# Optimization experiments

Measured on AMD Instinct MI355X. Metric: run time of the kernel, lower is better.

Reference implementation:

```python
import jax, jax.numpy as jnp
import numpy as np
from math import sqrt

BS, SEQ, NV, DM, K = 16, 1024, 512, 256, 8
EPS = 0.05  # sinkhorn epsilon
TEMP = 0.07  # concrete-bernoulli temperature


def setup_inputs() -> dict:
    key = jax.random.key(0)
    k1, k2, k3 = jax.random.split(key, 3)
    x = jax.random.normal(k1, (BS, SEQ, NV), jnp.float32)
    # nn.Linear(seq_len, d_model): weight [d_model, seq_len], bias [d_model]
    W = jax.random.normal(k2, (DM, SEQ), jnp.float32) / sqrt(SEQ)
    b = jnp.zeros((DM,), jnp.float32)
    cluster_emb = jax.random.normal(k3, (K, DM), jnp.float32) / sqrt(DM)
    return {"x": x, "W": W, "b": b, "cluster_emb": cluster_emb}


def _l2norm(z):
    # F.normalize(x, dim=1, p=2) with eps=1e-12 clamp
    n = jnp.maximum(jnp.linalg.norm(z, axis=1, keepdims=True), 1e-12)
    return z / n


def _sinkhorn(q):
    Q = jnp.exp(q / EPS)
    return Q / jnp.sum(Q, axis=1, keepdims=True)


def _concrete_bern(p, key):
    u = jax.random.uniform(key, p.shape, p.dtype, 1e-10, 1.0 - 1e-10)
    noise = jnp.log(u) - jnp.log1p(-u)
    logit = jnp.log(p + 1e-10) - jnp.log(1.0 - p + 1e-10)
    return jax.nn.sigmoid((logit + noise) / TEMP)


def _forward(x, W, b, cluster_emb):
    bs, S, nv = x.shape
    d = W.shape[0]
    k = cluster_emb.shape[0]
    # permute -> [bs, nv, S], Linear(S -> d)
    x_emb = jnp.einsum('bsv,ds->bvd', x, W) + b  # [bs, nv, d]
    x_flat = x_emb.reshape(-1, d)  # [bs*nv, d]
    # cosine-similarity cluster logits
    prob = (_l2norm(x_flat) @ _l2norm(cluster_emb).T).reshape(bs, nv, k)
    prob_temp = _sinkhorn(prob.reshape(-1, k)).reshape(bs, nv, k)  # individual probs
    prob_avg = _sinkhorn(jnp.mean(prob, axis=0))  # [nv, k]
    mask = _concrete_bern(prob_avg, jax.random.key(42))  # [nv, k]
    # CrossAttention with n_heads=1 (dropout inactive in eval)
    scale = 1.0 / sqrt(d)
    scores = jnp.einsum('kd,bvd->bkv', cluster_emb, x_emb)  # [bs, k, nv]
    A = jax.nn.softmax(scale * scores, axis=-1) * mask.T[None]  # masked attn
    V = jnp.einsum('bkv,bvd->bkd', A, x_emb)  # [bs, k, d]
    cluster_emb_avg = jnp.mean(V, axis=0)  # [k, d] (stored attribute in torch)
    # cluster_base_encoding: straight-through bernoulli, broadcast over seq_len
    soft = prob_temp.transpose(2, 0, 1)[..., None]  # [k, bs, nv, 1]
    u = jax.random.uniform(jax.random.key(7), soft.shape, soft.dtype)
    bern = (u < jax.lax.stop_gradient(soft)).astype(soft.dtype)
    extend = jnp.broadcast_to(bern, (k, bs, nv, S))  # [k, bs, nv, S]
    hard = soft + jax.lax.stop_gradient(extend - soft)  # straight-through
    return hard


def reference(x, W, b, cluster_emb):
    return _forward(x, W, b, cluster_emb)
```

## Files before the change

### kernel.cpp

```cpp
#include <hip/hip_runtime.h>
#include <math.h>
#include <stdint.h>

#define BS 16
#define SEQ 1024
#define NV 512
#define DM 256
#define NK 8

__device__ double g_WC[NK * SEQ];
__device__ double g_Bk[NK];
__device__ __align__(16) float g_Wt[SEQ * DM];
__device__ __align__(16) float g_zp[4 * BS * NV * DM];
__device__ double g_nn2[BS * NV];
__device__ double g_Dp[8 * BS * NV * NK];
__device__ unsigned char g_bits[BS * NV];

__device__ __forceinline__ void threefry2x32_key7(uint32_t x0, uint32_t x1,
                                                  uint32_t& o0, uint32_t& o1) {
    const uint32_t k0 = 0u, k1 = 7u;
    const uint32_t k2 = k0 ^ k1 ^ 0x1BD11BDAu;
    uint32_t v0 = x0 + k0, v1 = x1 + k1;
#define TF_ROUND(r) { v0 += v1; v1 = (v1 << (r)) | (v1 >> (32 - (r))); v1 ^= v0; }
    TF_ROUND(13) TF_ROUND(15) TF_ROUND(26) TF_ROUND(6)
    v0 += k1; v1 += k2 + 1u;
    TF_ROUND(17) TF_ROUND(29) TF_ROUND(16) TF_ROUND(24)
    v0 += k2; v1 += k0 + 2u;
    TF_ROUND(13) TF_ROUND(15) TF_ROUND(26) TF_ROUND(6)
    v0 += k0; v1 += k1 + 3u;
    TF_ROUND(17) TF_ROUND(29) TF_ROUND(16) TF_ROUND(24)
    v0 += k1; v1 += k2 + 4u;
    TF_ROUND(13) TF_ROUND(15) TF_ROUND(26) TF_ROUND(6)
    v0 += k2; v1 += k0 + 5u;
#undef TF_ROUND
    o0 = v0; o1 = v1;
}

__device__ __forceinline__ float bits_to_uniform(uint32_t b) {
    return __uint_as_float((b >> 9) | 0x3F800000u) - 1.0f;
}

__device__ __forceinline__ void cp16(const float* g, float* l) {
    __builtin_amdgcn_global_load_lds(
        (const __attribute__((address_space(1))) void*)g,
        (__attribute__((address_space(3))) void*)l,
        16, 0, 0);
}

__global__ __launch_bounds__(256) void prep_merged_kernel(
        const float* __restrict__ W, const float* __restrict__ bias,
        const float* __restrict__ ce) {
    __shared__ float tile[64][132];
    __shared__ double red[256];
    __shared__ double cen[256];
    const int t = threadIdx.x;
    const int bid = blockIdx.x;

    if (bid < 32) {
        const int s0 = (bid & 15) * 64;
        const int d0 = (bid >> 4) * 128;
#pragma unroll
        for (int p = 0; p < 32; ++p) {
            int lin = p * 256 + t;
            int d = lin >> 6, s = lin & 63;
            tile[s][d] = W[(size_t)(d0 + d) * SEQ + s0 + s];
        }
        __syncthreads();
#pragma unroll
        for (int p = 0; p < 32; ++p) {
            int lin = p * 256 + t;
            int s = lin >> 7, d = lin & 127;
            g_Wt[(size_t)(s0 + s) * DM + d0 + d] = tile[s][d];
        }
        return;
    }

    const int pid = bid - 32;
    const int k = pid >> 2;
    const int schunk = pid & 3;

    double c = (double)ce[k * DM + t];
    red[t] = c * c;
    __syncthreads();
    for (int off = 128; off > 0; off >>= 1) {
        if (t < off) red[t] += red[t + off];
        __syncthreads();
    }
    double nc = fmax(sqrt(red[0]), 1e-12);
    cen[t] = c / nc;
    __syncthreads();
    red[t] = (double)bias[t] * cen[t];
    __syncthreads();
    for (int off = 128; off > 0; off >>= 1) {
        if (t < off) red[t] += red[t + off];
        __syncthreads();
    }
    if (t == 0 && schunk == 0) g_Bk[k] = red[0];

    const int s = schunk * 256 + t;
    double acc = 0.0;
#pragma unroll 8
    for (int d = 0; d < DM; ++d)
        acc += cen[d] * (double)W[(size_t)d * SEQ + s];
    g_WC[(size_t)k * SEQ + s] = acc;
}

#define KC 32

__global__ __launch_bounds__(256) void gemm_kernel(
        const float* __restrict__ x) {
    __shared__ __align__(16) float wst[2][KC * 256];

    const int t = threadIdx.x;
    const int kblk = blockIdx.x;
    const int vblk = blockIdx.y;
    const int b    = blockIdx.z;
    const int v0 = vblk * 64;
    const float* xb = x + (size_t)b * SEQ * NV + v0;

    const int tv8 = (t & 7) * 8;
    const int td8 = (t >> 3) * 8;
    const int w = t >> 6;
    const int l = t & 63;

    const int wrow0 = w * 8;
    const size_t g_lane4 = (size_t)l * 4;

    float acc[8][8];
#pragma unroll
    for (int j = 0; j < 8; ++j)
#pragma unroll
        for (int i = 0; i < 8; ++i) acc[j][i] = 0.0f;

#define STAGE(BUF, S0)                                                         \
    {                                                                          \
        _Pragma("unroll")                                                      \
        for (int j = 0; j < 8; ++j) {                                          \
            int row = wrow0 + j;                                               \
            cp16(&g_Wt[(size_t)((S0) + row) * DM + g_lane4],                   \
                 &wst[BUF][row * 256]);                                        \
        }                                                                      \
    }

    const int sbeg = kblk * 256;

    STAGE(0, sbeg)
    __syncthreads();

    for (int c = 0; c < 8; ++c) {
        const int buf = c & 1;
        if (c < 7) STAGE(buf ^ 1, sbeg + (c + 1) * KC)

        const float* xrow = &xb[(size_t)(sbeg + c * KC) * NV + tv8];
#pragma unroll
        for (int kk = 0; kk < KC; ++kk) {
            const float* wr = &wst[buf][kk * 256 + td8];
            float4 xv0 = *(const float4*)(xrow);
            float4 xv1 = *(const float4*)(xrow + 4);
            float4 wv0 = *(const float4*)(wr);
            float4 wv1 = *(const float4*)(wr + 4);
            float xv[8] = {xv0.x, xv0.y, xv0.z, xv0.w, xv1.x, xv1.y, xv1.z, xv1.w};
            float wv[8] = {wv0.x, wv0.y, wv0.z, wv0.w, wv1.x, wv1.y, wv1.z, wv1.w};
#pragma unroll
            for (int j = 0; j < 8; ++j)
#pragma unroll
                for (int i = 0; i < 8; ++i) acc[j][i] += xv[j] * wv[i];
            xrow += NV;
        }

        __syncthreads();
    }
#undef STAGE

#pragma unroll
    for (int j = 0; j < 8; ++j) {
        size_t base = (size_t)kblk * (BS * NV * DM) +
                      ((size_t)b * NV + v0 + tv8 + j) * DM + td8;
#pragma unroll
        for (int m = 0; m < 8; m += 4)
            *(float4*)&g_zp[base + m] =
                make_float4(acc[j][m], acc[j][m + 1], acc[j][m + 2], acc[j][m + 3]);
    }
}

__global__ __launch_bounds__(256) void cd_kernel(
        const float* __restrict__ bias, const float* __restrict__ x) {
    __shared__ double sm[3072];
    const int t = threadIdx.x;
    const int bid = blockIdx.x;

    if (bid < 512) {
        const int vg = bid >> 4;
        const int b  = bid & 15;
        const int vl = t >> 4, dg = t & 15;
        const int v = vg * 16 + vl;

        const size_t bvbase = ((size_t)b * NV + v) * DM + dg * 16;
        double sq = 0.0;
#pragma unroll
        for (int m = 0; m < 16; m += 4) {
            float4 p0 = *(const float4*)&g_zp[(size_t)0 * (BS * NV * DM) + bvbase + m];
            float4 p1 = *(const float4*)&g_zp[(size_t)1 * (BS * NV * DM) + bvbase + m];
            float4 p2 = *(const float4*)&g_zp[(size_t)2 * (BS * NV * DM) + bvbase + m];
            float4 p3 = *(const float4*)&g_zp[(size_t)3 * (BS * NV * DM) + bvbase + m];
            float4 bb = *(const float4*)&bias[dg * 16 + m];
            double z0 = (double)p0.x + (double)p1.x + (double)p2.x + (double)p3.x + (double)bb.x;
            double z1 = (double)p0.y + (double)p1.y + (double)p2.y + (double)p3.y + (double)bb.y;
            double z2 = (double)p0.z + (double)p1.z + (double)p2.z + (double)p3.z + (double)bb.z;
            double z3 = (double)p0.w + (double)p1.w + (double)p2.w + (double)p3.w + (double)bb.w;
            sq += z0 * z0 + z1 * z1 + z2 * z2 + z3 * z3;
        }
        sm[vl * 17 + dg] = sq;
        __syncthreads();
        if (dg == 0) {
            double s = 0.0;
#pragma unroll
            for (int i = 0; i < 16; ++i) s += sm[vl * 17 + i];
            g_nn2[b * NV + v] = s;
        }
        return;
    }

    const int did  = bid - 512;
    const int vblk = did & 7;
    const int b    = (did >> 3) & 15;
    const int sc   = did >> 7;
    const int v0 = vblk * 64;
    const int ss = sc * 128;

    double* wcd = sm;
    double* dw  = sm + 1024;

#pragma unroll
    for (int j = 0; j < 4; ++j) {
        int idx = j * 256 + t;
        wcd[idx] = g_WC[(size_t)(idx >> 7) * SEQ + ss + (idx & 127)];
    }
    __syncthreads();

    const int vl = t & 63, w = t >> 6;
    const float* xp = x + (size_t)b * SEQ * NV + v0 + vl;
    double D[NK];
#pragma unroll
    for (int k = 0; k < NK; ++k) D[k] = 0.0;
    const int sw = w * 32;
    for (int i = 0; i < 32; ++i) {
        int sl = sw + i;
        double xv = (double)xp[(size_t)(ss + sl) * NV];
#pragma unroll
        for (int k = 0; k < NK; ++k) D[k] += xv * wcd[k * 128 + sl];
    }
#pragma unroll
    for (int k = 0; k < NK; ++k) dw[(w * 64 + vl) * NK + k] = D[k];
    __syncthreads();

    const int v = t & 63, k2 = (t >> 6) * 2;
#pragma unroll
    for (int j = 0; j < 2; ++j) {
        int k = k2 + j;
        double s = dw[(0 * 64 + v) * NK + k] + dw[(1 * 64 + v) * NK + k] +
                   dw[(2 * 64 + v) * NK + k] + dw[(3 * 64 + v) * NK + k];
        g_Dp[(((size_t)sc * BS + b) * NV + v0 + v) * NK + k] = s;
    }
}

__global__ __launch_bounds__(256) void finalize_kernel() {
    const int bv = blockIdx.x * 256 + threadIdx.x;
    double n = fmax(sqrt(g_nn2[bv]), 1e-12);

    double D[NK];
#pragma unroll
    for (int k = 0; k < NK; ++k) D[k] = g_Bk[k];
#pragma unroll
    for (int sc = 0; sc < 8; ++sc) {
#pragma unroll
        for (int k = 0; k < NK; ++k)
            D[k] += g_Dp[((size_t)sc * (BS * NV) + bv) * NK + k];
    }

    double p[NK], sum = 0.0;
#pragma unroll
    for (int k = 0; k < NK; ++k) {
        p[k] = exp((D[k] / n) / 0.05);
        sum += p[k];
    }
    unsigned int byte = 0;
#pragma unroll
    for (int k = 0; k < NK; ++k) {
        uint32_t i = (uint32_t)(k * (BS * NV) + bv);
        uint32_t y0, y1;
        threefry2x32_key7(0u, i, y0, y1);
        float u = bits_to_uniform(y0 ^ y1);
        if ((double)u < p[k] / sum) byte |= 1u << k;
    }
    g_bits[bv] = (unsigned char)byte;
}

__global__ __launch_bounds__(256) void write_kernel(float* __restrict__ out) {
    const int t = threadIdx.x;
    const size_t r0 = (size_t)blockIdx.x * 8;
#pragma unroll
    for (int j = 0; j < 8; ++j) {
        size_t r = r0 + j;
        unsigned int bv = (unsigned int)(r & 8191u);
        unsigned int k  = (unsigned int)(r >> 13);
        float v = ((g_bits[bv] >> k) & 1u) ? 1.0f : 0.0f;
        float4 val = make_float4(v, v, v, v);
        ((float4*)(out + r * 1024))[t] = val;
    }
}

extern "C" void kernel_launch(void* const* d_in, const int* in_sizes, int n_in,
                              void* d_out, int out_size, void* d_ws, size_t ws_size,
                              hipStream_t stream) {
    const float* x    = (const float*)d_in[0];
    const float* W    = (const float*)d_in[1];
    const float* bias = (const float*)d_in[2];
    const float* ce   = (const float*)d_in[3];
    float* out = (float*)d_out;

    prep_merged_kernel<<<dim3(64), dim3(256), 0, stream>>>(W, bias, ce);
    gemm_kernel<<<dim3(4, 8, 16), dim3(256), 0, stream>>>(x);
    cd_kernel<<<dim3(1536), dim3(256), 0, stream>>>(bias, x);
    finalize_kernel<<<dim3(32), dim3(256), 0, stream>>>();
    write_kernel<<<dim3(8192), dim3(256), 0, stream>>>(out);
}
```

Before: 419.2 us.

## Retile GEMM into single-wave blocks staging both x and W in LDS

```diff
diff --git a/kernel.cpp b/kernel.cpp
--- a/kernel.cpp
+++ b/kernel.cpp
@@ -70,7 +70,8 @@
         for (int p = 0; p < 32; ++p) {
             int lin = p * 256 + t;
             int s = lin >> 7, d = lin & 127;
-            g_Wt[(size_t)(s0 + s) * DM + d0 + d] = tile[s][d];
+            int D = d0 + d;
+            g_Wt[((size_t)(D >> 6) * SEQ + s0 + s) * 64 + (D & 63)] = tile[s][d];
         }
         return;
     }
@@ -105,26 +106,28 @@
     g_WC[(size_t)k * SEQ + s] = acc;
 }
 
-#define KC 32
-
-__global__ __launch_bounds__(256) void gemm_kernel(
+#define KC 16
+
+__global__ __launch_bounds__(64) void gemm_kernel(
         const float* __restrict__ x) {
-    __shared__ __align__(16) float wst[2][KC * 256];
-
-    const int t = threadIdx.x;
-    const int kblk = blockIdx.x;
+    __shared__ __align__(16) float xs[2][KC * 64];
+    __shared__ __align__(16) float wst[2][KC * 64];
+
+    const int l = threadIdx.x;
+    const int kblk = blockIdx.x & 3;
+    const int dblk = blockIdx.x >> 2;
     const int vblk = blockIdx.y;
     const int b    = blockIdx.z;
     const int v0 = vblk * 64;
     const float* xb = x + (size_t)b * SEQ * NV + v0;
-
-    const int tv8 = (t & 7) * 8;
-    const int td8 = (t >> 3) * 8;
-    const int w = t >> 6;
-    const int l = t & 63;
-
-    const int wrow0 = w * 8;
-    const size_t g_lane4 = (size_t)l * 4;
+    const float* wb = g_Wt + (size_t)dblk * SEQ * 64;
+
+    const int tv8 = (l & 7) * 8;
+    const int td8 = (l >> 3) * 8;
+
+    const int l4   = l * 4;
+    const int xrs  = l >> 4;
+    const int xcol = (l & 15) * 4;
 
     float acc[8][8];
 #pragma unroll
@@ -135,28 +138,30 @@
 #define STAGE(BUF, S0)                                                         \
     {                                                                          \
         _Pragma("unroll")                                                      \
-        for (int j = 0; j < 8; ++j) {                                          \
-            int row = wrow0 + j;                                               \
-            cp16(&g_Wt[(size_t)((S0) + row) * DM + g_lane4],                   \
-                 &wst[BUF][row * 256]);                                        \
-        }                                                                      \
+        for (int j = 0; j < 4; ++j)                                            \
+            cp16(&wb[(size_t)((S0) + j * 4) * 64 + l4], &wst[BUF][j * 256]);   \
+        _Pragma("unroll")                                                      \
+        for (int j = 0; j < 4; ++j)                                            \
+            cp16(&xb[(size_t)((S0) + j * 4 + xrs) * NV + xcol],                \
+                 &xs[BUF][j * 256]);                                           \
     }
 
     const int sbeg = kblk * 256;
 
     STAGE(0, sbeg)
-    __syncthreads();
-
-    for (int c = 0; c < 8; ++c) {
+    asm volatile("s_waitcnt vmcnt(0) lgkmcnt(0)" ::: "memory");
+    __builtin_amdgcn_sched_barrier(0);
+
+    for (int c = 0; c < 16; ++c) {
         const int buf = c & 1;
-        if (c < 7) STAGE(buf ^ 1, sbeg + (c + 1) * KC)
-
-        const float* xrow = &xb[(size_t)(sbeg + c * KC) * NV + tv8];
+        if (c < 15) STAGE(buf ^ 1, sbeg + (c + 1) * KC)
+
 #pragma unroll
         for (int kk = 0; kk < KC; ++kk) {
-            const float* wr = &wst[buf][kk * 256 + td8];
-            float4 xv0 = *(const float4*)(xrow);
-            float4 xv1 = *(const float4*)(xrow + 4);
+            const float* xr = &xs[buf][kk * 64 + tv8];
+            const float* wr = &wst[buf][kk * 64 + td8];
+            float4 xv0 = *(const float4*)(xr);
+            float4 xv1 = *(const float4*)(xr + 4);
             float4 wv0 = *(const float4*)(wr);
             float4 wv1 = *(const float4*)(wr + 4);
             float xv[8] = {xv0.x, xv0.y, xv0.z, xv0.w, xv1.x, xv1.y, xv1.z, xv1.w};
@@ -165,17 +170,17 @@
             for (int j = 0; j < 8; ++j)
 #pragma unroll
                 for (int i = 0; i < 8; ++i) acc[j][i] += xv[j] * wv[i];
-            xrow += NV;
-        }
-
-        __syncthreads();
+        }
+
+        asm volatile("s_waitcnt vmcnt(0) lgkmcnt(0)" ::: "memory");
+        __builtin_amdgcn_sched_barrier(0);
     }
 #undef STAGE
 
 #pragma unroll
     for (int j = 0; j < 8; ++j) {
         size_t base = (size_t)kblk * (BS * NV * DM) +
-                      ((size_t)b * NV + v0 + tv8 + j) * DM + td8;
+                      ((size_t)b * NV + v0 + tv8 + j) * DM + dblk * 64 + td8;
 #pragma unroll
         for (int m = 0; m < 8; m += 4)
             *(float4*)&g_zp[base + m] =
@@ -320,7 +325,7 @@
     float* out = (float*)d_out;
 
     prep_merged_kernel<<<dim3(64), dim3(256), 0, stream>>>(W, bias, ce);
-    gemm_kernel<<<dim3(4, 8, 16), dim3(256), 0, stream>>>(x);
+    gemm_kernel<<<dim3(16, 8, 16), dim3(64), 0, stream>>>(x);
     cd_kernel<<<dim3(1536), dim3(256), 0, stream>>>(bias, x);
     finalize_kernel<<<dim3(32), dim3(256), 0, stream>>>();
     write_kernel<<<dim3(8192), dim3(256), 0, stream>>>(out);
```

Measured after the change: 401.8 us. 4.1% less time.

## Stage x tiles through LDS with triple-buffered async pipeline in GEMM

Applied to the files above, without the earlier changes.

```diff
diff --git a/kernel.cpp b/kernel.cpp
--- a/kernel.cpp
+++ b/kernel.cpp
@@ -105,11 +105,12 @@
     g_WC[(size_t)k * SEQ + s] = acc;
 }
 
-#define KC 32
+#define KC 16
 
 __global__ __launch_bounds__(256) void gemm_kernel(
         const float* __restrict__ x) {
-    __shared__ __align__(16) float wst[2][KC * 256];
+    __shared__ __align__(16) float xs[3][KC * 64];
+    __shared__ __align__(16) float wst[3][KC * 256];
 
     const int t = threadIdx.x;
     const int kblk = blockIdx.x;
@@ -123,8 +124,10 @@
     const int w = t >> 6;
     const int l = t & 63;
 
-    const int wrow0 = w * 8;
-    const size_t g_lane4 = (size_t)l * 4;
+    const int l4  = l * 4;
+    const int xr4 = l >> 4;
+    const int xc4 = (l & 15) * 4;
+    const int wrow0 = w * 4;
 
     float acc[8][8];
 #pragma unroll
@@ -132,45 +135,66 @@
 #pragma unroll
         for (int i = 0; i < 8; ++i) acc[j][i] = 0.0f;
 
-#define STAGE(BUF, S0)                                                         \
+    const int sbeg = kblk * 256;
+
+#define STAGE(BUF, C)                                                          \
     {                                                                          \
+        const int S0 = sbeg + (C) * KC;                                        \
         _Pragma("unroll")                                                      \
-        for (int j = 0; j < 8; ++j) {                                          \
-            int row = wrow0 + j;                                               \
-            cp16(&g_Wt[(size_t)((S0) + row) * DM + g_lane4],                   \
-                 &wst[BUF][row * 256]);                                        \
-        }                                                                      \
-    }
-
-    const int sbeg = kblk * 256;
-
-    STAGE(0, sbeg)
-    __syncthreads();
-
-    for (int c = 0; c < 8; ++c) {
-        const int buf = c & 1;
-        if (c < 7) STAGE(buf ^ 1, sbeg + (c + 1) * KC)
-
-        const float* xrow = &xb[(size_t)(sbeg + c * KC) * NV + tv8];
-#pragma unroll
-        for (int kk = 0; kk < KC; ++kk) {
-            const float* wr = &wst[buf][kk * 256 + td8];
-            float4 xv0 = *(const float4*)(xrow);
-            float4 xv1 = *(const float4*)(xrow + 4);
-            float4 wv0 = *(const float4*)(wr);
-            float4 wv1 = *(const float4*)(wr + 4);
-            float xv[8] = {xv0.x, xv0.y, xv0.z, xv0.w, xv1.x, xv1.y, xv1.z, xv1.w};
-            float wv[8] = {wv0.x, wv0.y, wv0.z, wv0.w, wv1.x, wv1.y, wv1.z, wv1.w};
-#pragma unroll
-            for (int j = 0; j < 8; ++j)
-#pragma unroll
-                for (int i = 0; i < 8; ++i) acc[j][i] += xv[j] * wv[i];
-            xrow += NV;
-        }
-
-        __syncthreads();
-    }
+        for (int j = 0; j < 4; ++j)                                            \
+            cp16(&g_Wt[(size_t)(S0 + wrow0 + j) * DM + l4],                    \
+                 &wst[BUF][(wrow0 + j) * 256]);                                \
+        cp16(&xb[(size_t)(S0 + wrow0 + xr4) * NV + xc4],                       \
+             &xs[BUF][wrow0 * 64]);                                            \
+    }
+
+#define MAC(BUF)                                                               \
+    _Pragma("unroll")                                                          \
+    for (int kk = 0; kk < KC; ++kk) {                                          \
+        const float* xr = &xs[BUF][kk * 64 + tv8];                             \
+        const float* wr = &wst[BUF][kk * 256 + td8];                           \
+        float4 xv0 = *(const float4*)(xr);                                     \
+        float4 xv1 = *(const float4*)(xr + 4);                                 \
+        float4 wv0 = *(const float4*)(wr);                                     \
+        float4 wv1 = *(const float4*)(wr + 4);                                 \
+        float xv[8] = {xv0.x, xv0.y, xv0.z, xv0.w, xv1.x, xv1.y, xv1.z, xv1.w};\
+        float wv[8] = {wv0.x, wv0.y, wv0.z, wv0.w, wv1.x, wv1.y, wv1.z, wv1.w};\
+        _Pragma("unroll")                                                      \
+        for (int j = 0; j < 8; ++j)                                            \
+            _Pragma("unroll")                                                  \
+            for (int i = 0; i < 8; ++i) acc[j][i] += xv[j] * wv[i];            \
+    }
+
+#define VMW(N)                                                                 \
+    asm volatile("s_waitcnt vmcnt(" #N ")" ::: "memory");                      \
+    __builtin_amdgcn_sched_barrier(0);
+
+#define BAR()                                                                  \
+    __builtin_amdgcn_s_barrier();                                              \
+    __builtin_amdgcn_sched_barrier(0);
+
+    STAGE(0, 0)
+    STAGE(1, 1)
+
+    for (int c = 0; c < 14; ++c) {
+        STAGE((c + 2) % 3, c + 2)
+        VMW(10)
+        BAR()
+        MAC(c % 3)
+        BAR()
+    }
+    VMW(5)
+    BAR()
+    MAC(2)
+    BAR()
+    VMW(0)
+    BAR()
+    MAC(0)
+
 #undef STAGE
+#undef MAC
+#undef VMW
+#undef BAR
 
 #pragma unroll
     for (int j = 0; j < 8; ++j) {
```

After: 405.0 us. 1.04x faster.

## Replace FP32 FMA GEMM with 3-way bf16-split MFMA GEMM

Applied to the files above, without the earlier changes.

```diff
diff --git a/kernel.cpp b/kernel.cpp
--- a/kernel.cpp
+++ b/kernel.cpp
@@ -8,9 +8,17 @@
 #define DM 256
 #define NK 8
 
+typedef __attribute__((ext_vector_type(8))) short bf16x8;
+typedef __attribute__((ext_vector_type(4))) float f32x4;
+
 __device__ double g_WC[NK * SEQ];
 __device__ double g_Bk[NK];
-__device__ __align__(16) float g_Wt[SEQ * DM];
+__device__ __align__(16) unsigned short g_x0[BS * NV * SEQ];
+__device__ __align__(16) unsigned short g_x1[BS * NV * SEQ];
+__device__ __align__(16) unsigned short g_x2[BS * NV * SEQ];
+__device__ __align__(16) unsigned short g_w0[DM * SEQ];
+__device__ __align__(16) unsigned short g_w1[DM * SEQ];
+__device__ __align__(16) unsigned short g_w2[DM * SEQ];
 __device__ __align__(16) float g_zp[4 * BS * NV * DM];
 __device__ double g_nn2[BS * NV];
 __device__ double g_Dp[8 * BS * NV * NK];
@@ -40,44 +48,63 @@
     return __uint_as_float((b >> 9) | 0x3F800000u) - 1.0f;
 }
 
-__device__ __forceinline__ void cp16(const float* g, float* l) {
+__device__ __forceinline__ unsigned short f2bf(float f) {
+    uint32_t u = __float_as_uint(f);
+    return (unsigned short)((u + 0x7FFFu + ((u >> 16) & 1u)) >> 16);
+}
+__device__ __forceinline__ float bf2f(unsigned short h) {
+    return __uint_as_float(((uint32_t)h) << 16);
+}
+__device__ __forceinline__ void split3(float f, unsigned short& h0,
+                                       unsigned short& h1, unsigned short& h2) {
+    h0 = f2bf(f);
+    float r1 = f - bf2f(h0);
+    h1 = f2bf(r1);
+    float r2 = r1 - bf2f(h1);
+    h2 = f2bf(r2);
+}
+
+__device__ __forceinline__ void cp16s(const unsigned short* g, unsigned short* l) {
     __builtin_amdgcn_global_load_lds(
         (const __attribute__((address_space(1))) void*)g,
         (__attribute__((address_space(3))) void*)l,
         16, 0, 0);
 }
 
-__global__ __launch_bounds__(256) void prep_merged_kernel(
+__global__ __launch_bounds__(256) void prep_kernel(
         const float* __restrict__ W, const float* __restrict__ bias,
         const float* __restrict__ ce) {
-    __shared__ float tile[64][132];
     __shared__ double red[256];
     __shared__ double cen[256];
     const int t = threadIdx.x;
     const int bid = blockIdx.x;
 
-    if (bid < 32) {
-        const int s0 = (bid & 15) * 64;
-        const int d0 = (bid >> 4) * 128;
-#pragma unroll
-        for (int p = 0; p < 32; ++p) {
-            int lin = p * 256 + t;
-            int d = lin >> 6, s = lin & 63;
-            tile[s][d] = W[(size_t)(d0 + d) * SEQ + s0 + s];
-        }
-        __syncthreads();
-#pragma unroll
-        for (int p = 0; p < 32; ++p) {
-            int lin = p * 256 + t;
-            int s = lin >> 7, d = lin & 127;
-            g_Wt[(size_t)(s0 + s) * DM + d0 + d] = tile[s][d];
-        }
+    if (bid >= 32) {
+        const int base = (bid - 32) * 4096 + t * 16;
+        uint32_t p0[8], p1[8], p2[8];
+#pragma unroll
+        for (int i = 0; i < 16; ++i) {
+            unsigned short h0, h1, h2;
+            split3(W[base + i], h0, h1, h2);
+            if (i & 1) {
+                p0[i >> 1] |= (uint32_t)h0 << 16;
+                p1[i >> 1] |= (uint32_t)h1 << 16;
+                p2[i >> 1] |= (uint32_t)h2 << 16;
+            } else {
+                p0[i >> 1] = h0; p1[i >> 1] = h1; p2[i >> 1] = h2;
+            }
+        }
+        *(uint4*)&g_w0[base]     = make_uint4(p0[0], p0[1], p0[2], p0[3]);
+        *(uint4*)&g_w0[base + 8] = make_uint4(p0[4], p0[5], p0[6], p0[7]);
+        *(uint4*)&g_w1[base]     = make_uint4(p1[0], p1[1], p1[2], p1[3]);
+        *(uint4*)&g_w1[base + 8] = make_uint4(p1[4], p1[5], p1[6], p1[7]);
+        *(uint4*)&g_w2[base]     = make_uint4(p2[0], p2[1], p2[2], p2[3]);
+        *(uint4*)&g_w2[base + 8] = make_uint4(p2[4], p2[5], p2[6], p2[7]);
         return;
     }
 
-    const int pid = bid - 32;
-    const int k = pid >> 2;
-    const int schunk = pid & 3;
+    const int k = bid >> 2;
+    const int schunk = bid & 3;
 
     double c = (double)ce[k * DM + t];
     red[t] = c * c;
@@ -105,82 +132,126 @@
     g_WC[(size_t)k * SEQ + s] = acc;
 }
 
-#define KC 32
-
-__global__ __launch_bounds__(256) void gemm_kernel(
-        const float* __restrict__ x) {
-    __shared__ __align__(16) float wst[2][KC * 256];
-
-    const int t = threadIdx.x;
-    const int kblk = blockIdx.x;
+__global__ __launch_bounds__(256) void xsplit_kernel(const float* __restrict__ x) {
+    __shared__ float tile[64][65];
+    const int t = threadIdx.x;
+    const int stile = blockIdx.x >> 3, vtile = blockIdx.x & 7;
+    const int b = blockIdx.y;
+    const int s0 = stile * 64, v0 = vtile * 64;
+    const float* xb = x + ((size_t)b * SEQ + s0) * NV + v0;
+
+#pragma unroll
+    for (int p = 0; p < 16; ++p) {
+        int lin = p * 256 + t;
+        int sl = lin >> 6, vv = lin & 63;
+        tile[sl][vv] = xb[(size_t)sl * NV + vv];
+    }
+    __syncthreads();
+
+    const int vr = t >> 2, g = t & 3;
+    const size_t obase = ((size_t)b * NV + v0 + vr) * SEQ + s0 + g * 16;
+    uint32_t p0[8], p1[8], p2[8];
+#pragma unroll
+    for (int i = 0; i < 16; ++i) {
+        unsigned short h0, h1, h2;
+        split3(tile[g * 16 + i][vr], h0, h1, h2);
+        if (i & 1) {
+            p0[i >> 1] |= (uint32_t)h0 << 16;
+            p1[i >> 1] |= (uint32_t)h1 << 16;
+            p2[i >> 1] |= (uint32_t)h2 << 16;
+        } else {
+            p0[i >> 1] = h0; p1[i >> 1] = h1; p2[i >> 1] = h2;
+        }
+    }
+    *(uint4*)&g_x0[obase]     = make_uint4(p0[0], p0[1], p0[2], p0[3]);
+    *(uint4*)&g_x0[obase + 8] = make_uint4(p0[4], p0[5], p0[6], p0[7]);
+    *(uint4*)&g_x1[obase]     = make_uint4(p1[0], p1[1], p1[2], p1[3]);
+    *(uint4*)&g_x1[obase + 8] = make_uint4(p1[4], p1[5], p1[6], p1[7]);
+    *(uint4*)&g_x2[obase]     = make_uint4(p2[0], p2[1], p2[2], p2[3]);
+    *(uint4*)&g_x2[obase + 8] = make_uint4(p2[4], p2[5], p2[6], p2[7]);
+}
+
+__global__ __launch_bounds__(256) void gemm_kernel() {
+    __shared__ __align__(16) unsigned short xs3[3][64 * 32];
+    __shared__ __align__(16) unsigned short ws3[3][128 * 32];
+
+    const int t = threadIdx.x;
+    const int kblk = blockIdx.x & 3;
+    const int dblk = blockIdx.x >> 2;
     const int vblk = blockIdx.y;
     const int b    = blockIdx.z;
-    const int v0 = vblk * 64;
-    const float* xb = x + (size_t)b * SEQ * NV + v0;
-
-    const int tv8 = (t & 7) * 8;
-    const int td8 = (t >> 3) * 8;
-    const int w = t >> 6;
-    const int l = t & 63;
-
-    const int wrow0 = w * 8;
-    const size_t g_lane4 = (size_t)l * 4;
-
-    float acc[8][8];
-#pragma unroll
-    for (int j = 0; j < 8; ++j)
-#pragma unroll
-        for (int i = 0; i < 8; ++i) acc[j][i] = 0.0f;
-
-#define STAGE(BUF, S0)                                                         \
-    {                                                                          \
-        _Pragma("unroll")                                                      \
-        for (int j = 0; j < 8; ++j) {                                          \
-            int row = wrow0 + j;                                               \
-            cp16(&g_Wt[(size_t)((S0) + row) * DM + g_lane4],                   \
-                 &wst[BUF][row * 256]);                                        \
-        }                                                                      \
-    }
-
-    const int sbeg = kblk * 256;
-
-    STAGE(0, sbeg)
-    __syncthreads();
+    const int v0 = vblk * 64, d0 = dblk * 128;
+    const int w = t >> 6, l = t & 63;
+
+    const int srow = l >> 2;
+    const int sk8  = ((l & 3) ^ ((l >> 2) & 3)) * 8;
+    const int rrow = l & 15;
+    const int rsl  = ((l >> 4) ^ (l & 3)) * 8;
+
+    const size_t xbase = ((size_t)b * NV + v0) * SEQ;
+    const size_t wbase = (size_t)d0 * SEQ;
+    const unsigned short* xsrc[3] = {g_x0 + xbase, g_x1 + xbase, g_x2 + xbase};
+    const unsigned short* wsrc[3] = {g_w0 + wbase, g_w1 + wbase, g_w2 + wbase};
+
+    f32x4 acc[4][2];
+#pragma unroll
+    for (int mb = 0; mb < 4; ++mb)
+#pragma unroll
+        for (int nb = 0; nb < 2; ++nb) acc[mb][nb] = (f32x4){0.f, 0.f, 0.f, 0.f};
 
     for (int c = 0; c < 8; ++c) {
-        const int buf = c & 1;
-        if (c < 7) STAGE(buf ^ 1, sbeg + (c + 1) * KC)
-
-        const float* xrow = &xb[(size_t)(sbeg + c * KC) * NV + tv8];
-#pragma unroll
-        for (int kk = 0; kk < KC; ++kk) {
-            const float* wr = &wst[buf][kk * 256 + td8];
-            float4 xv0 = *(const float4*)(xrow);
-            float4 xv1 = *(const float4*)(xrow + 4);
-            float4 wv0 = *(const float4*)(wr);
-            float4 wv1 = *(const float4*)(wr + 4);
-            float xv[8] = {xv0.x, xv0.y, xv0.z, xv0.w, xv1.x, xv1.y, xv1.z, xv1.w};
-            float wv[8] = {wv0.x, wv0.y, wv0.z, wv0.w, wv1.x, wv1.y, wv1.z, wv1.w};
-#pragma unroll
-            for (int j = 0; j < 8; ++j)
-#pragma unroll
-                for (int i = 0; i < 8; ++i) acc[j][i] += xv[j] * wv[i];
-            xrow += NV;
-        }
-
-        __syncthreads();
-    }
-#undef STAGE
-
-#pragma unroll
-    for (int j = 0; j < 8; ++j) {
-        size_t base = (size_t)kblk * (BS * NV * DM) +
-                      ((size_t)b * NV + v0 + tv8 + j) * DM + td8;
-#pragma unroll
-        for (int m = 0; m < 8; m += 4)
-            *(float4*)&g_zp[base + m] =
-                make_float4(acc[j][m], acc[j][m + 1], acc[j][m + 2], acc[j][m + 3]);
-    }
+        const int s0 = kblk * 256 + c * 32;
+        __syncthreads();
+#pragma unroll
+        for (int sp = 0; sp < 3; ++sp) {
+            cp16s(&xsrc[sp][(size_t)(w * 16 + srow) * SEQ + s0 + sk8],
+                  &xs3[sp][w * 16 * 32]);
+            cp16s(&wsrc[sp][(size_t)(w * 32 + srow) * SEQ + s0 + sk8],
+                  &ws3[sp][w * 32 * 32]);
+            cp16s(&wsrc[sp][(size_t)(w * 32 + 16 + srow) * SEQ + s0 + sk8],
+                  &ws3[sp][(w * 32 + 16) * 32]);
+        }
+        __syncthreads();
+
+        bf16x8 a[3][4], bb[3][2];
+#pragma unroll
+        for (int sp = 0; sp < 3; ++sp) {
+#pragma unroll
+            for (int mb = 0; mb < 4; ++mb)
+                a[sp][mb] = *(const bf16x8*)&xs3[sp][(mb * 16 + rrow) * 32 + rsl];
+#pragma unroll
+            for (int nb = 0; nb < 2; ++nb)
+                bb[sp][nb] = *(const bf16x8*)
+                    &ws3[sp][(w * 32 + nb * 16 + rrow) * 32 + rsl];
+        }
+#pragma unroll
+        for (int mb = 0; mb < 4; ++mb)
+#pragma unroll
+            for (int nb = 0; nb < 2; ++nb) {
+                f32x4 v = acc[mb][nb];
+                v = __builtin_amdgcn_mfma_f32_16x16x32_bf16(a[1][mb], bb[1][nb], v, 0, 0, 0);
+                v = __builtin_amdgcn_mfma_f32_16x16x32_bf16(a[0][mb], bb[2][nb], v, 0, 0, 0);
+                v = __builtin_amdgcn_mfma_f32_16x16x32_bf16(a[2][mb], bb[0][nb], v, 0, 0, 0);
+                v = __builtin_amdgcn_mfma_f32_16x16x32_bf16(a[0][mb], bb[1][nb], v, 0, 0, 0);
+                v = __builtin_amdgcn_mfma_f32_16x16x32_bf16(a[1][mb], bb[0][nb], v, 0, 0, 0);
+                v = __builtin_amdgcn_mfma_f32_16x16x32_bf16(a[0][mb], bb[0][nb], v, 0, 0, 0);
+                acc[mb][nb] = v;
+            }
+    }
+
+    const int rowb = (l >> 4) * 4;
+#pragma unroll
+    for (int mb = 0; mb < 4; ++mb)
+#pragma unroll
+        for (int nb = 0; nb < 2; ++nb) {
+            const int d = d0 + w * 32 + nb * 16 + (l & 15);
+#pragma unroll
+            for (int r = 0; r < 4; ++r) {
+                const int v = v0 + mb * 16 + rowb + r;
+                g_zp[(size_t)kblk * (BS * NV * DM) +
+                     ((size_t)b * NV + v) * DM + d] = acc[mb][nb][r];
+            }
+        }
 }
 
 __global__ __launch_bounds__(256) void cd_kernel(
@@ -319,8 +390,9 @@
     const float* ce   = (const float*)d_in[3];
     float* out = (float*)d_out;
 
-    prep_merged_kernel<<<dim3(64), dim3(256), 0, stream>>>(W, bias, ce);
-    gemm_kernel<<<dim3(4, 8, 16), dim3(256), 0, stream>>>(x);
+    prep_kernel<<<dim3(96), dim3(256), 0, stream>>>(W, bias, ce);
+    xsplit_kernel<<<dim3(128, 16), dim3(256), 0, stream>>>(x);
+    gemm_kernel<<<dim3(8, 8, 16), dim3(256), 0, stream>>>();
     cd_kernel<<<dim3(1536), dim3(256), 0, stream>>>(bias, x);
     finalize_kernel<<<dim3(32), dim3(256), 0, stream>>>();
     write_kernel<<<dim3(8192), dim3(256), 0, stream>>>(out);
```

Result: faster. 392.6 us (-6.4%).
